# Performance work log

Measured on AMD Instinct MI355X. Metric: run time of the kernel, lower is better.

## Reference

```python
import jax, jax.numpy as jnp
import numpy as np
import math

B, S, D, H = 4, 1024, 1024, 16
DK = D // H


def setup_inputs() -> dict:
    key = jax.random.key(0)
    ks = jax.random.split(key, 12)
    scale = 1.0 / math.sqrt(D)
    inp = {
        "query": jax.random.normal(ks[0], (B, S, D), jnp.float32),
        "key": jax.random.normal(ks[1], (B, S, D), jnp.float32),
        "value": jax.random.normal(ks[2], (B, S, D), jnp.float32),
        "mask": jnp.ones((B, S, S), jnp.int32),
        "Wq": jax.random.uniform(ks[3], (D, D), jnp.float32, -scale, scale),
        "bq": jax.random.uniform(ks[4], (D,), jnp.float32, -scale, scale),
        "Wk": jax.random.uniform(ks[5], (D, D), jnp.float32, -scale, scale),
        "bk": jax.random.uniform(ks[6], (D,), jnp.float32, -scale, scale),
        "Wv": jax.random.uniform(ks[7], (D, D), jnp.float32, -scale, scale),
        "bv": jax.random.uniform(ks[8], (D,), jnp.float32, -scale, scale),
        "Wo": jax.random.uniform(ks[9], (D, D), jnp.float32, -scale, scale),
        "bo": jax.random.uniform(ks[10], (D,), jnp.float32, -scale, scale),
    }
    return inp


def reference(query, key, value, mask, Wq, bq, Wk, bk, Wv, bv, Wo, bo):
    b, s, d = query.shape
    # QKV projections (torch Linear: x @ W.T + b), split into heads -> [b, h, s, dk]
    def proj(x, W, bias):
        return (x @ W.T + bias).reshape(b, -1, H, DK).transpose(0, 2, 1, 3)

    q = proj(query, Wq, bq)
    k = proj(key, Wk, bk)
    v = proj(value, Wv, bv)

    scores = jnp.einsum("bhqd,bhkd->bhqk", q, k) / jnp.sqrt(jnp.float32(DK))
    scores = jnp.where(mask[:, None, :, :] == 0, jnp.float32(-1e9), scores)
    p_attn = jax.nn.softmax(scores, axis=-1)  # dropout p=0.0 -> identity

    x = jnp.einsum("bhqk,bhkd->bhqd", p_attn, v)
    x = x.transpose(0, 2, 1, 3).reshape(b, -1, H * DK)  # [b, s, d]
    # F.threshold(x, 0.2, 0.0): values <= 0.2 replaced with 0
    x = jnp.where(x > 0.2, x, jnp.float32(0.0))
    x1 = x @ Wo.T + bo
    x1 = jnp.mean(x1, axis=-1, keepdims=True)
    return x + x1
```

## Files before the change

### kernel.cpp

```cpp
#include <hip/hip_runtime.h>
#include <hip/hip_bf16.h>
#include <math.h>

#define BB 4
#define SS 1024
#define DD 1024
#define NH 16
#define DKH 64

typedef __attribute__((ext_vector_type(8))) short bf16x8;
typedef __attribute__((ext_vector_type(4))) float f32x4;
typedef __attribute__((ext_vector_type(16))) float f32x16;

__device__ __forceinline__ ushort f2bf(float f) {
  __hip_bfloat16 h = __float2bfloat16(f);
  return *(ushort*)&h;
}

__device__ __forceinline__ bf16x8 pack8(float4 a, float4 b) {
  bf16x8 r;
  r[0] = (short)f2bf(a.x); r[1] = (short)f2bf(a.y);
  r[2] = (short)f2bf(a.z); r[3] = (short)f2bf(a.w);
  r[4] = (short)f2bf(b.x); r[5] = (short)f2bf(b.y);
  r[6] = (short)f2bf(b.z); r[7] = (short)f2bf(b.w);
  return r;
}

__device__ __forceinline__ void async16(const void* g, void* l) {
  __builtin_amdgcn_global_load_lds(
      (const __attribute__((address_space(1))) unsigned int*)g,
      (__attribute__((address_space(3))) unsigned int*)l, 16, 0, 0);
}

__global__ __launch_bounds__(256) void prep_all(
    const float* __restrict__ Xq, const float* __restrict__ Xk, const float* __restrict__ Xv,
    const int* __restrict__ mask,
    const float* __restrict__ Wq, const float* __restrict__ Wk, const float* __restrict__ Wv,
    const float* __restrict__ Wo, const float* __restrict__ bo,
    ushort* __restrict__ Wb, ushort* __restrict__ Ab,
    float* __restrict__ wo_sum, float* __restrict__ bo_mean,
    int* __restrict__ maskOK) {
  __shared__ int smi[4];
  const int bid = blockIdx.x;
  const int tid = threadIdx.x;

  if (bid < 64) {
    const int row0 = bid * 16;
    float4 acc = make_float4(0.f, 0.f, 0.f, 0.f);
#pragma unroll
    for (int r = 0; r < 16; ++r) {
      const float4 v = *(const float4*)(Wo + (size_t)(row0 + r) * DD + tid * 4);
      acc.x += v.x; acc.y += v.y; acc.z += v.z; acc.w += v.w;
    }
    atomicAdd(&wo_sum[tid * 4 + 0], acc.x);
    atomicAdd(&wo_sum[tid * 4 + 1], acc.y);
    atomicAdd(&wo_sum[tid * 4 + 2], acc.z);
    atomicAdd(&wo_sum[tid * 4 + 3], acc.w);
    return;
  }

  if (bid == 64) {
    if (tid < 64) {
      float s = 0.f;
      for (int i = tid; i < 1024; i += 64) s += bo[i];
#pragma unroll
      for (int off = 1; off < 64; off <<= 1) s += __shfl_xor(s, off);
      if (tid == 0) *bo_mean = s * (1.0f / 1024.0f);
    }
    return;
  }

  if (bid < 577) {
    const int m = bid - 65;
    const int kt = m & 15, qt = (m >> 4) & 7, b = m >> 7;
    const int row = tid >> 1, half = tid & 1;
    const int* p = mask + ((size_t)b * SS + qt * 128 + row) * SS + kt * 64 + half * 32;
    int ok = 1;
#pragma unroll
    for (int j = 0; j < 8; ++j) {
      const int4 mm = *(const int4*)(p + j * 4);
      ok &= (mm.x != 0) & (mm.y != 0) & (mm.z != 0) & (mm.w != 0);
    }
    const unsigned long long bal = __ballot(ok);
    if ((tid & 63) == 0) smi[tid >> 6] = (bal == ~0ULL) ? 1 : 0;
    __syncthreads();
    if (tid == 0) maskOK[(b * 8 + qt) * 16 + kt] = smi[0] & smi[1] & smi[2] & smi[3];
    return;
  }

  if (bid < 1345) {
    const int c0 = bid - 577;
#pragma unroll
    for (int it = 0; it < 8; ++it) {
      const size_t g = (size_t)(c0 + it * 768) * 2048 + (size_t)tid * 8;
      const int t = (int)(g >> 22);
      const float* base = (t == 0) ? Xq : (t == 1) ? Xk : Xv;
      const size_t off = g & 4194303;
      const float4 f0 = *(const float4*)(base + off);
      const float4 f1 = *(const float4*)(base + off + 4);
      *(bf16x8*)(Ab + g) = pack8(f0, f1);
    }
    return;
  }

  {
    const int c0 = bid - 1345;
#pragma unroll
    for (int it = 0; it < 8; ++it) {
      const size_t g = (size_t)(c0 + it * 192) * 2048 + (size_t)tid * 8;
      const int t = (int)(g >> 20);
      const float* W = (t == 0) ? Wq : (t == 1) ? Wk : Wv;
      const size_t off = g & 1048575;
      const float4 f0 = *(const float4*)(W + off);
      const float4 f1 = *(const float4*)(W + off + 4);
      *(bf16x8*)(Wb + g) = pack8(f0, f1);
    }
  }
}

__global__ __launch_bounds__(256) void gemm_qkv_bf16(
    const ushort* __restrict__ Ab, const ushort* __restrict__ Wb,
    const float* __restrict__ bq, const float* __restrict__ bk, const float* __restrict__ bv,
    ushort* __restrict__ QKVb) {
  const int z = blockIdx.z;
  const char* A = (const char*)(Ab + (size_t)z * 4194304);
  const char* W = (const char*)(Wb + (size_t)z * 1048576);
  const float* bias = (z == 0) ? bq : (z == 1) ? bk : bv;
  ushort* Cz = QKVb + (size_t)z * 4194304;
  const float scale = (z == 0) ? 0.125f : 1.0f;

  __shared__ ushort As[8192];
  __shared__ ushort Ws[8192];

  const int tid = threadIdx.x;
  const int lane = tid & 63, w = tid >> 6;
  const int l31 = lane & 31, kh = lane >> 5;
  const int wn = w & 1, wm = w >> 1;
  const int m0 = blockIdx.x * 128, n0 = blockIdx.y * 128;

  const int r8 = lane >> 3;
  const int cg = (lane & 7) ^ r8;
  const int xr = l31 & 7;

  f32x16 acc[2][2];
#pragma unroll
  for (int mt = 0; mt < 2; ++mt)
#pragma unroll
    for (int nt = 0; nt < 2; ++nt)
#pragma unroll
      for (int r = 0; r < 16; ++r) acc[mt][nt][r] = 0.f;

  for (int k0 = 0; k0 < DD; k0 += 64) {
    __syncthreads();
#pragma unroll
    for (int t = 0; t < 4; ++t) {
      const int grp = w * 4 + t;
      const int row = grp * 8 + r8;
      async16(A + ((size_t)(m0 + row) * DD + k0 + cg * 8) * 2, &As[grp * 512]);
      async16(W + ((size_t)(n0 + row) * DD + k0 + cg * 8) * 2, &Ws[grp * 512]);
    }
    __syncthreads();
#pragma unroll
    for (int ks = 0; ks < 4; ++ks) {
      const int sc = (ks * 2 + kh) ^ xr;
      bf16x8 wf[2], af[2];
#pragma unroll
      for (int nt = 0; nt < 2; ++nt)
        wf[nt] = *(const bf16x8*)&Ws[(wn * 64 + nt * 32 + l31) * 64 + sc * 8];
#pragma unroll
      for (int mt = 0; mt < 2; ++mt)
        af[mt] = *(const bf16x8*)&As[(wm * 64 + mt * 32 + l31) * 64 + sc * 8];
#pragma unroll
      for (int mt = 0; mt < 2; ++mt)
#pragma unroll
        for (int nt = 0; nt < 2; ++nt)
          acc[mt][nt] = __builtin_amdgcn_mfma_f32_32x32x16_bf16(wf[nt], af[mt], acc[mt][nt], 0, 0, 0);
    }
  }

#pragma unroll
  for (int nt = 0; nt < 2; ++nt) {
#pragma unroll
    for (int g = 0; g < 4; ++g) {
      const int ng = n0 + wn * 64 + nt * 32 + kh * 4 + g * 8;
      const float4 b4 = *(const float4*)(bias + ng);
#pragma unroll
      for (int mt = 0; mt < 2; ++mt) {
        ushort4 pk;
        pk.x = f2bf((acc[mt][nt][g * 4 + 0] + b4.x) * scale);
        pk.y = f2bf((acc[mt][nt][g * 4 + 1] + b4.y) * scale);
        pk.z = f2bf((acc[mt][nt][g * 4 + 2] + b4.z) * scale);
        pk.w = f2bf((acc[mt][nt][g * 4 + 3] + b4.w) * scale);
        *(ushort4*)&Cz[(size_t)(m0 + wm * 64 + mt * 32 + l31) * DD + ng] = pk;
      }
    }
  }
}

__global__ __launch_bounds__(256) void flash_mfma(
    const ushort* __restrict__ QKVb, const int* __restrict__ mask,
    const int* __restrict__ maskOK, float* __restrict__ X) {
  __shared__ ushort Vt[64 * 72];
  __shared__ ushort Ps[128 * 72];

  const ushort* Qb = QKVb;
  const ushort* Kb = QKVb + 4194304;
  const ushort* Vb = QKVb + 8388608;

  const int tid = threadIdx.x;
  const int lane = tid & 63, w = tid >> 6;
  const int quad = lane >> 4, l15 = lane & 15;
  const int h = blockIdx.x, qblk = blockIdx.y, b = blockIdx.z;
  const int qbase = qblk * 128 + w * 32;

  bf16x8 qf[2][2];
#pragma unroll
  for (int qt = 0; qt < 2; ++qt)
#pragma unroll
    for (int ks = 0; ks < 2; ++ks)
      qf[qt][ks] = *(const bf16x8*)(Qb + (size_t)(b * SS + qbase + qt * 16 + l15) * DD +
                                    h * DKH + ks * 32 + quad * 8);

  f32x4 o[4][2];
  const f32x4 z4 = {0.f, 0.f, 0.f, 0.f};
#pragma unroll
  for (int dt = 0; dt < 4; ++dt)
#pragma unroll
    for (int qt = 0; qt < 2; ++qt) o[dt][qt] = z4;
  float l_run[2] = {0.f, 0.f};

  const int vp = tid & 31;
  const int vdc = tid >> 5;
  const ushort* Vg = Vb + (size_t)(b * SS) * DD + h * DKH + vdc * 8;
  const ushort* Kg = Kb + (size_t)(b * SS) * DD + h * DKH;
  uint* VtU = (uint*)Vt;
  const int* Mb = mask + (size_t)b * SS * SS;

  for (int kt = 0; kt < 16; ++kt) {
    const int k064 = kt * 64;
    __syncthreads();

    bf16x8 kf[4][2];
#pragma unroll
    for (int mt = 0; mt < 4; ++mt)
#pragma unroll
      for (int ks = 0; ks < 2; ++ks)
        kf[mt][ks] = *(const bf16x8*)(Kg + (size_t)(k064 + mt * 16 + l15) * DD +
                                      ks * 32 + quad * 8);

    union { uint4 u; ushort s[8]; } v0, v1;
    v0.u = *(const uint4*)(Vg + (size_t)(k064 + 2 * vp) * DD);
    v1.u = *(const uint4*)(Vg + (size_t)(k064 + 2 * vp + 1) * DD);
#pragma unroll
    for (int j = 0; j < 8; ++j)
      VtU[(vdc * 8 + j) * 36 + vp] = (uint)v0.s[j] | ((uint)v1.s[j] << 16);
    __syncthreads();

    f32x4 s[4][2];
#pragma unroll
    for (int mt = 0; mt < 4; ++mt)
#pragma unroll
      for (int qt = 0; qt < 2; ++qt) {
        f32x4 a = z4;
        a = __builtin_amdgcn_mfma_f32_16x16x32_bf16(kf[mt][0], qf[qt][0], a, 0, 0, 0);
        a = __builtin_amdgcn_mfma_f32_16x16x32_bf16(kf[mt][1], qf[qt][1], a, 0, 0, 0);
        s[mt][qt] = a;
      }

    const int ok = maskOK[(b * 8 + qblk) * 16 + kt];
    if (!ok) {
#pragma unroll
      for (int mt = 0; mt < 4; ++mt)
#pragma unroll
        for (int qt = 0; qt < 2; ++qt)
#pragma unroll
          for (int reg = 0; reg < 4; ++reg) {
            const int q = qbase + qt * 16 + l15;
            const int key = k064 + mt * 16 + quad * 4 + reg;
            if (Mb[(size_t)q * SS + key] == 0) s[mt][qt][reg] = -1e9f;
          }
    }

#pragma unroll
    for (int qt = 0; qt < 2; ++qt) {
      float rs = 0.f;
#pragma unroll
      for (int mt = 0; mt < 4; ++mt) {
#pragma unroll
        for (int reg = 0; reg < 4; ++reg) {
          const float p = __expf(s[mt][qt][reg]);
          s[mt][qt][reg] = p;
          rs += p;
        }
      }
      l_run[qt] += rs;
#pragma unroll
      for (int mt = 0; mt < 4; ++mt) {
        ushort4 pk;
        pk.x = f2bf(s[mt][qt][0]);
        pk.y = f2bf(s[mt][qt][1]);
        pk.z = f2bf(s[mt][qt][2]);
        pk.w = f2bf(s[mt][qt][3]);
        *(ushort4*)&Ps[(w * 32 + qt * 16 + l15) * 72 + mt * 16 + quad * 4] = pk;
      }
    }

    bf16x8 pf[2][2];
#pragma unroll
    for (int qt = 0; qt < 2; ++qt)
#pragma unroll
      for (int ks = 0; ks < 2; ++ks)
        pf[qt][ks] = *(const bf16x8*)&Ps[(w * 32 + qt * 16 + l15) * 72 + ks * 32 + quad * 8];
#pragma unroll
    for (int dt = 0; dt < 4; ++dt) {
      bf16x8 vf0 = *(const bf16x8*)&Vt[(dt * 16 + l15) * 72 + quad * 8];
      bf16x8 vf1 = *(const bf16x8*)&Vt[(dt * 16 + l15) * 72 + 32 + quad * 8];
#pragma unroll
      for (int qt = 0; qt < 2; ++qt) {
        o[dt][qt] = __builtin_amdgcn_mfma_f32_16x16x32_bf16(vf0, pf[qt][0], o[dt][qt], 0, 0, 0);
        o[dt][qt] = __builtin_amdgcn_mfma_f32_16x16x32_bf16(vf1, pf[qt][1], o[dt][qt], 0, 0, 0);
      }
    }
  }

#pragma unroll
  for (int qt = 0; qt < 2; ++qt) {
    float l = l_run[qt];
    l += __shfl_xor(l, 16);
    l += __shfl_xor(l, 32);
    const float inv = 1.0f / l;
#pragma unroll
    for (int dt = 0; dt < 4; ++dt) {
      const f32x4 ov = o[dt][qt] * inv;
      *(f32x4*)(X + (size_t)(b * SS + qbase + qt * 16 + l15) * DD +
                h * DKH + dt * 16 + quad * 4) = ov;
    }
  }
}

__global__ __launch_bounds__(256) void epilogue_kernel(float* __restrict__ X,
                                                       const float* __restrict__ wo_sum,
                                                       const float* __restrict__ bo_mean) {
  __shared__ float red[4][4];
  const int tid = threadIdx.x;
  const float4 wv = *(const float4*)(wo_sum + tid * 4);
  const float bm = *bo_mean;
  float4 xt[4];
#pragma unroll
  for (int r = 0; r < 4; ++r) {
    const int row = blockIdx.x * 4 + r;
    const float4 x = *(const float4*)(X + (size_t)row * DD + tid * 4);
    xt[r].x = (x.x > 0.2f) ? x.x : 0.f;
    xt[r].y = (x.y > 0.2f) ? x.y : 0.f;
    xt[r].z = (x.z > 0.2f) ? x.z : 0.f;
    xt[r].w = (x.w > 0.2f) ? x.w : 0.f;
    float part = xt[r].x * wv.x + xt[r].y * wv.y + xt[r].z * wv.z + xt[r].w * wv.w;
#pragma unroll
    for (int off = 1; off < 64; off <<= 1) part += __shfl_xor(part, off);
    if ((tid & 63) == 0) red[r][tid >> 6] = part;
  }
  __syncthreads();
#pragma unroll
  for (int r = 0; r < 4; ++r) {
    const int row = blockIdx.x * 4 + r;
    const float x1 = ((red[r][0] + red[r][1]) + (red[r][2] + red[r][3])) * (1.0f / 1024.0f) + bm;
    const float4 o = make_float4(xt[r].x + x1, xt[r].y + x1, xt[r].z + x1, xt[r].w + x1);
    *(float4*)(X + (size_t)row * DD + tid * 4) = o;
  }
}

extern "C" void kernel_launch(void* const* d_in, const int* in_sizes, int n_in,
                              void* d_out, int out_size, void* d_ws, size_t ws_size,
                              hipStream_t stream) {
  const float* Xq = (const float*)d_in[0];
  const float* Xk = (const float*)d_in[1];
  const float* Xv = (const float*)d_in[2];
  const int* mask = (const int*)d_in[3];
  const float* Wq = (const float*)d_in[4];
  const float* bq = (const float*)d_in[5];
  const float* Wk = (const float*)d_in[6];
  const float* bk = (const float*)d_in[7];
  const float* Wv = (const float*)d_in[8];
  const float* bv = (const float*)d_in[9];
  const float* Wo = (const float*)d_in[10];
  const float* bo = (const float*)d_in[11];

  ushort* Wb = (ushort*)d_ws;
  ushort* Ab = Wb + (size_t)3 * 1048576;
  ushort* QKVb = Ab + (size_t)3 * 4194304;
  float* wo_sum = (float*)(QKVb + (size_t)3 * 4194304);
  float* bo_mean = wo_sum + 1024;
  int* maskOK = (int*)(bo_mean + 1);
  float* X = (float*)d_out;

  hipMemsetAsync(wo_sum, 0, 1024 * sizeof(float), stream);

  prep_all<<<1537, 256, 0, stream>>>(Xq, Xk, Xv, mask, Wq, Wk, Wv, Wo, bo,
                                     Wb, Ab, wo_sum, bo_mean, maskOK);

  gemm_qkv_bf16<<<dim3(32, 8, 3), 256, 0, stream>>>(Ab, Wb, bq, bk, bv, QKVb);

  flash_mfma<<<dim3(16, 8, 4), 256, 0, stream>>>(QKVb, mask, maskOK, X);

  epilogue_kernel<<<1024, 256, 0, stream>>>(X, wo_sum, bo_mean);
}
```

Measured before the change: 224.6 us.

## Prefetch next K/V tile into registers and raise MFMA wave priority

The attention loop now loads the next iteration's K fragments and V rows into registers while the current tile is computed, so global-load latency overlaps the MFMA work. The V transpose into shared memory uses the prefetched registers, bracketed by raw barriers and an explicit lgkmcnt wait. s_setprio is raised around both MFMA blocks to favour matrix issue. This costs extra VGPRs for the double-buffered fragments, which may reduce occupancy, and the last iteration issues a redundant load of tile 0.

Result: faster. 218.5 us (-2.7%).

```diff
diff --git a/kernel.cpp b/kernel.cpp
--- a/kernel.cpp
+++ b/kernel.cpp
@@ -236,27 +236,43 @@
   uint* VtU = (uint*)Vt;
   const int* Mb = mask + (size_t)b * SS * SS;
 
+  union U8 { uint4 u; ushort s[8]; };
+
+  bf16x8 kf[4][2];
+#pragma unroll
+  for (int mt = 0; mt < 4; ++mt)
+#pragma unroll
+    for (int ks = 0; ks < 2; ++ks)
+      kf[mt][ks] = *(const bf16x8*)(Kg + (size_t)(mt * 16 + l15) * DD + ks * 32 + quad * 8);
+  U8 v0c, v1c;
+  v0c.u = *(const uint4*)(Vg + (size_t)(2 * vp) * DD);
+  v1c.u = *(const uint4*)(Vg + (size_t)(2 * vp + 1) * DD);
+
   for (int kt = 0; kt < 16; ++kt) {
     const int k064 = kt * 64;
-    __syncthreads();
-
-    bf16x8 kf[4][2];
+
+    __builtin_amdgcn_s_barrier();
+#pragma unroll
+    for (int j = 0; j < 8; ++j)
+      VtU[(vdc * 8 + j) * 36 + vp] = (uint)v0c.s[j] | ((uint)v1c.s[j] << 16);
+    asm volatile("s_waitcnt lgkmcnt(0)" ::: "memory");
+    __builtin_amdgcn_sched_barrier(0);
+    __builtin_amdgcn_s_barrier();
+
+    const int kn = (kt < 15) ? (k064 + 64) : 0;
+    bf16x8 kfn[4][2];
 #pragma unroll
     for (int mt = 0; mt < 4; ++mt)
 #pragma unroll
       for (int ks = 0; ks < 2; ++ks)
-        kf[mt][ks] = *(const bf16x8*)(Kg + (size_t)(k064 + mt * 16 + l15) * DD +
-                                      ks * 32 + quad * 8);
-
-    union { uint4 u; ushort s[8]; } v0, v1;
-    v0.u = *(const uint4*)(Vg + (size_t)(k064 + 2 * vp) * DD);
-    v1.u = *(const uint4*)(Vg + (size_t)(k064 + 2 * vp + 1) * DD);
-#pragma unroll
-    for (int j = 0; j < 8; ++j)
-      VtU[(vdc * 8 + j) * 36 + vp] = (uint)v0.s[j] | ((uint)v1.s[j] << 16);
-    __syncthreads();
+        kfn[mt][ks] = *(const bf16x8*)(Kg + (size_t)(kn + mt * 16 + l15) * DD +
+                                       ks * 32 + quad * 8);
+    U8 v0n, v1n;
+    v0n.u = *(const uint4*)(Vg + (size_t)(kn + 2 * vp) * DD);
+    v1n.u = *(const uint4*)(Vg + (size_t)(kn + 2 * vp + 1) * DD);
 
     f32x4 s[4][2];
+    __builtin_amdgcn_s_setprio(1);
 #pragma unroll
     for (int mt = 0; mt < 4; ++mt)
 #pragma unroll
@@ -266,6 +282,7 @@
         a = __builtin_amdgcn_mfma_f32_16x16x32_bf16(kf[mt][1], qf[qt][1], a, 0, 0, 0);
         s[mt][qt] = a;
       }
+    __builtin_amdgcn_s_setprio(0);
 
     const int ok = maskOK[(b * 8 + qblk) * 16 + kt];
     if (!ok) {
@@ -311,6 +328,7 @@
 #pragma unroll
       for (int ks = 0; ks < 2; ++ks)
         pf[qt][ks] = *(const bf16x8*)&Ps[(w * 32 + qt * 16 + l15) * 72 + ks * 32 + quad * 8];
+    __builtin_amdgcn_s_setprio(1);
 #pragma unroll
     for (int dt = 0; dt < 4; ++dt) {
       bf16x8 vf0 = *(const bf16x8*)&Vt[(dt * 16 + l15) * 72 + quad * 8];
@@ -321,6 +339,15 @@
         o[dt][qt] = __builtin_amdgcn_mfma_f32_16x16x32_bf16(vf1, pf[qt][1], o[dt][qt], 0, 0, 0);
       }
     }
+    __builtin_amdgcn_s_setprio(0);
+
+#pragma unroll
+    for (int mt = 0; mt < 4; ++mt)
+#pragma unroll
+      for (int ks = 0; ks < 2; ++ks)
+        kf[mt][ks] = kfn[mt][ks];
+    v0c.u = v0n.u;
+    v1c.u = v1n.u;
   }
 
 #pragma unroll
```
